# Performance work log

Measured on AMD Instinct MI355X. Metric: run time of the kernel, lower is better.

## Reference

```python
import jax, jax.numpy as jnp
import numpy as np

B, CIN, COUT, H, W = 16, 128, 128, 64, 64
E, PS, FF = 8, 16, 8
GC, HID, HC = 4 * FF, 64, COUT * 4  # gate_channel, gate hidden, bottleneck hidden


def conv(x, w, stride=1, pad=0, groups=1):
    # x: [B,C,H,W], w: [O,I/groups,kh,kw]
    return jax.lax.conv_general_dilated(
        x, w, (stride, stride), [(pad, pad), (pad, pad)], feature_group_count=groups)


def group_norm(x, scale, bias, groups, eps=1e-5):
    b, c = x.shape[:2]
    xr = x.reshape(b, groups, c // groups, *x.shape[2:])
    m = xr.mean(axis=(2, 3, 4), keepdims=True)
    v = xr.var(axis=(2, 3, 4), keepdims=True)
    xr = (xr - m) * jax.lax.rsqrt(v + eps)
    return xr.reshape(x.shape) * scale[None, :, None, None] + bias[None, :, None, None]


def setup_inputs() -> dict:
    key = jax.random.key(0)
    ks = jax.random.split(key, 8)
    f = lambda k, shp: jax.random.normal(k, shp, jnp.float32) * 0.05
    return dict(
        x=jax.random.normal(ks[0], (B, CIN, H, W), jnp.float32),
        w_exp=f(ks[1], (E, COUT, CIN, 3, 3)),
        gn_exp_s=jnp.ones((E, COUT), jnp.float32),
        gn_exp_b=jnp.zeros((E, COUT), jnp.float32),
        w1=f(ks[2], (GC, HID)), b1=jnp.zeros((HID,), jnp.float32),
        w2=f(ks[3], (HID, E)), b2=jnp.zeros((E,), jnp.float32),
        w_pw1=f(ks[4], (HC, COUT, 1, 1)),
        gn1_s=jnp.ones((HC,), jnp.float32), gn1_b=jnp.zeros((HC,), jnp.float32),
        w_dw=f(ks[5], (HC, 1, 3, 3)),
        gn2_s=jnp.ones((HC,), jnp.float32), gn2_b=jnp.zeros((HC,), jnp.float32),
        w_pw2=f(ks[6], (COUT, HC, 1, 1)),
        gn3_s=jnp.ones((COUT,), jnp.float32), gn3_b=jnp.zeros((COUT,), jnp.float32),
    )


def reference(x, w_exp, gn_exp_s, gn_exp_b, w1, b1, w2, b2,
              w_pw1, gn1_s, gn1_b, w_dw, gn2_s, gn2_b, w_pw2, gn3_s, gn3_b):
    # ---- Conv experts (residual 3x3 conv + GN + SiLU), vmapped over experts ----
    def expert(w, s, b):
        y = conv(x, w, pad=1)
        y = group_norm(y, s, b, groups=min(8, COUT))
        return jax.nn.silu(y) + x  # use_residual=True, CIN == COUT

    ys = jax.vmap(expert)(w_exp, gn_exp_s, gn_exp_b)  # [E,B,C,H,W]

    # ---- Router gate: Fourier features of patch-center coordinates ----
    ph, pw = H // PS, W // PS
    cy = (jnp.arange(ph, dtype=jnp.float32) + 0.5) / ph
    cx = (jnp.arange(pw, dtype=jnp.float32) + 0.5) / pw
    freqs = (2.0 ** jnp.arange(FF, dtype=jnp.float32)) * jnp.pi
    ay = cy[:, None] * freqs  # [ph,FF]
    ax = cx[:, None] * freqs  # [pw,FF]
    feats = jnp.concatenate([
        jnp.broadcast_to(jnp.sin(ay)[:, None, :], (ph, pw, FF)),
        jnp.broadcast_to(jnp.cos(ay)[:, None, :], (ph, pw, FF)),
        jnp.broadcast_to(jnp.sin(ax)[None, :, :], (ph, pw, FF)),
        jnp.broadcast_to(jnp.cos(ax)[None, :, :], (ph, pw, FF)),
    ], axis=-1)  # [ph,pw,4*FF] == gate_channel
    hgate = jax.nn.silu(feats @ w1 + b1)
    wts = jax.nn.softmax(hgate @ w2 + b2, axis=-1)  # [ph,pw,E]

    # ---- Patch-wise combine of expert outputs ----
    wmap = jnp.repeat(jnp.repeat(wts, PS, axis=0), PS, axis=1)  # [H,W,E]
    combined = jnp.einsum('ebchw,hwe->bchw', ys, wmap)

    # ---- Inverted bottleneck: 1x1 -> dw3x3 -> 1x1(stride2) with GN+SiLU ----
    h = jax.nn.silu(group_norm(conv(combined, w_pw1), gn1_s, gn1_b, groups=8))
    h = jax.nn.silu(group_norm(conv(h, w_dw, pad=1, groups=HC), gn2_s, gn2_b, groups=8))
    h = jax.nn.silu(group_norm(conv(h, w_pw2, stride=2), gn3_s, gn3_b, groups=8))
    return h  # [B, COUT, H//2, W//2]
```

## Files before the change

kernel.cpp:

```cpp
#include <hip/hip_runtime.h>
#include <hip/hip_bf16.h>


#define B_ 16
#define CIN_ 128
#define COUT_ 128
#define H_ 64
#define W_ 64
#define HW_ 4096
#define E_ 8
#define FF_ 8
#define GC_ 32
#define HID_ 64
#define HC_ 512

typedef __hip_bfloat16 bf16;
typedef __bf16 bf16x8 __attribute__((ext_vector_type(8)));
typedef float f32x4 __attribute__((ext_vector_type(4)));

__device__ __forceinline__ float siluf(float v) { return v / (1.f + __expf(-v)); }
__device__ __forceinline__ float bf2f(bf16 v) { return __bfloat162float(v); }
__device__ __forceinline__ bf16 f2bf(float v) { return __float2bfloat16(v); }

__global__ void gate_kernel(const float* __restrict__ w1, const float* __restrict__ b1,
                            const float* __restrict__ w2, const float* __restrict__ b2,
                            float* __restrict__ wts) {
  int p = threadIdx.x;
  if (p >= 16) return;
  int i = p >> 2, j = p & 3;
  float cy = (i + 0.5f) * 0.25f;
  float cx = (j + 0.5f) * 0.25f;
  float feats[GC_];
#pragma unroll
  for (int f = 0; f < FF_; ++f) {
    float fr = 3.14159265358979f * (float)(1 << f);
    float ay = cy * fr, ax = cx * fr;
    feats[f] = sinf(ay);
    feats[FF_ + f] = cosf(ay);
    feats[2 * FF_ + f] = sinf(ax);
    feats[3 * FF_ + f] = cosf(ax);
  }
  float hid[HID_];
  for (int k = 0; k < HID_; ++k) {
    float a = b1[k];
#pragma unroll
    for (int m = 0; m < GC_; ++m) a = fmaf(feats[m], w1[m * HID_ + k], a);
    hid[k] = siluf(a);
  }
  float lg[E_];
  float mx = -1e30f;
#pragma unroll
  for (int e = 0; e < E_; ++e) {
    float a = b2[e];
    for (int k = 0; k < HID_; ++k) a = fmaf(hid[k], w2[k * E_ + e], a);
    lg[e] = a;
    mx = fmaxf(mx, a);
  }
  float s = 0.f;
#pragma unroll
  for (int e = 0; e < E_; ++e) { lg[e] = __expf(lg[e] - mx); s += lg[e]; }
  float inv = 1.f / s;
#pragma unroll
  for (int e = 0; e < E_; ++e) wts[p * E_ + e] = lg[e] * inv;
}

__global__ __launch_bounds__(256) void xt_kernel(const float* __restrict__ x,
                                                 bf16* __restrict__ xT) {
  __shared__ float t[128][65];
  int b = blockIdx.x >> 6, h = blockIdx.x & 63;
  int tid = threadIdx.x;
  int w = tid & 63, c4 = tid >> 6;
  const float* xb = x + ((size_t)(b * 128) * 64 + h) * 64;
#pragma unroll 4
  for (int rep = 0; rep < 32; ++rep) {
    int ci = rep * 4 + c4;
    t[ci][w] = xb[(size_t)ci * HW_ + w];
  }
  __syncthreads();
  bf16* dst = xT + (size_t)(b * 64 + h) * 8192;
#pragma unroll 4
  for (int rep = 0; rep < 32; ++rep) {
    int o = rep * 256 + tid;
    int cg = o >> 9, w2 = (o >> 3) & 63, lo = o & 7;
    dst[o] = f2bf(t[cg * 8 + lo][w2]);
  }
}

__global__ void wt_kernel(const float* __restrict__ w_exp, bf16* __restrict__ wT) {
  int idx = blockIdx.x * 256 + threadIdx.x;
  if (idx >= 1179648) return;
  int lo = idx & 7;
  int co = (idx >> 3) & 127;
  int cg = (idx >> 10) & 15;
  int rest = idx >> 14;
  int tap = rest % 9, e = rest / 9;
  int ci = cg * 8 + lo;
  wT[idx] = f2bf(w_exp[(((size_t)(e * 128 + co) * 128 + ci) * 9) + tap]);
}

__global__ void wpT_kernel(const float* __restrict__ w_pw1, const float* __restrict__ w_pw2,
                           bf16* __restrict__ wp1T, bf16* __restrict__ wp2T) {
  int idx = blockIdx.x * 256 + threadIdx.x;
  if (idx < 65536) wp1T[idx] = f2bf(w_pw1[idx]);
  else if (idx < 131072) wp2T[idx - 65536] = f2bf(w_pw2[idx - 65536]);
}

__global__ __launch_bounds__(256, 2) void conv_mfma(
    const bf16* __restrict__ xT, const bf16* __restrict__ wT,
    float* __restrict__ statsE, bf16* __restrict__ ys) {
  __shared__ __align__(16) char xls[8 * 6144];
  __shared__ __align__(16) char wls[8 * 2048];
  __shared__ float red[4][8][2];

  int blk = blockIdx.x;
  int rt = blk & 15, b = (blk >> 4) & 15, e = blk >> 8;
  int tid = threadIdx.x, lane = tid & 63, wave = tid >> 6;
  int quad = lane >> 4, l15 = lane & 15;
  int h0 = rt * 4;
  int h_local = wave;

  f32x4 acc[8][4];
#pragma unroll
  for (int mt = 0; mt < 8; ++mt)
#pragma unroll
    for (int nt = 0; nt < 4; ++nt) acc[mt][nt] = (f32x4){0.f, 0.f, 0.f, 0.f};

  bf16x8 bz;
#pragma unroll
  for (int j = 0; j < 8; ++j) bz[j] = (__bf16)0.f;

  for (int half = 0; half < 2; ++half) {
    __syncthreads();
#pragma unroll
    for (int s = 0; s < 12; ++s) {
      int seg = wave * 12 + s;
      int cg = seg / 6, r = seg % 6;
      int h = h0 - 1 + r;
      char* ldst = xls + cg * 6144 + r * 1024 + lane * 16;
      if ((unsigned)h < 64u) {
        const uint4* g = (const uint4*)((const char*)xT +
            ((size_t)((b * 64 + h) * 16) + half * 8 + cg) * 1024) + lane;
        *(uint4*)ldst = *g;
      } else {
        *(uint4*)ldst = make_uint4(0u, 0u, 0u, 0u);
      }
    }
    for (int tap = 0; tap < 9; ++tap) {
      int dr = tap / 3, ds = tap % 3;
      __syncthreads();
#pragma unroll
      for (int s = 0; s < 4; ++s) {
        int seg = wave * 4 + s;
        int cg = seg >> 1, cb = seg & 1;
        const uint4* g = (const uint4*)((const char*)wT +
            ((size_t)(((e * 9 + tap) * 16) + half * 8 + cg) * 128 + cb * 64) * 16) + lane;
        *(uint4*)(wls + cg * 2048 + cb * 1024 + lane * 16) = *g;
      }
      __syncthreads();
      int r_local = h_local + dr;
#pragma unroll
      for (int kc = 0; kc < 2; ++kc) {
        int cgq = kc * 4 + quad;
        bf16x8 af[8];
#pragma unroll
        for (int mt = 0; mt < 8; ++mt)
          af[mt] = *(const bf16x8*)(wls + cgq * 2048 + (mt * 16 + l15) * 16);
        bf16x8 bfr[4];
#pragma unroll
        for (int nt = 0; nt < 4; ++nt) {
          int w = nt * 16 + l15;
          int wsrc = w + ds - 1;
          bool valid = (unsigned)wsrc < 64u;
          int wc = valid ? wsrc : 0;
          bf16x8 v = *(const bf16x8*)(xls + cgq * 6144 + (r_local * 64 + wc) * 16);
          bfr[nt] = valid ? v : bz;
        }
#pragma unroll
        for (int mt = 0; mt < 8; ++mt)
#pragma unroll
          for (int nt = 0; nt < 4; ++nt)
            acc[mt][nt] = __builtin_amdgcn_mfma_f32_16x16x32_bf16(
                af[mt], bfr[nt], acc[mt][nt], 0, 0, 0);
      }
    }
  }

  int hh = h0 + h_local;
  bf16* yb = ys + (size_t)((e * 16 + b) * 128) * 4096;
#pragma unroll
  for (int mt = 0; mt < 8; ++mt) {
    float s = 0.f, ss = 0.f;
#pragma unroll
    for (int nt = 0; nt < 4; ++nt) {
      int w = nt * 16 + l15;
      int pos = hh * 64 + w;
#pragma unroll
      for (int r = 0; r < 4; ++r) {
        float v = acc[mt][nt][r];
        s += v;
        ss += v * v;
        int co = mt * 16 + quad * 4 + r;
        yb[(size_t)co * 4096 + pos] = f2bf(v);
      }
    }
#pragma unroll
    for (int off = 32; off; off >>= 1) {
      s += __shfl_down(s, off, 64);
      ss += __shfl_down(ss, off, 64);
    }
    if (lane == 0) { red[wave][mt][0] = s; red[wave][mt][1] = ss; }
  }
  __syncthreads();
  if (tid < 16) {
    int g = tid >> 1, which = tid & 1;
    float t = red[0][g][which] + red[1][g][which] + red[2][g][which] + red[3][g][which];
    atomicAdd(&statsE[((e * 16 + b) * 8 + g) * 2 + which], t);
  }
}

__global__ void finalize_stats(float* __restrict__ st, int n, float inv) {
  int i = blockIdx.x * 256 + threadIdx.x;
  if (i >= n) return;
  float S = st[i * 2], SS = st[i * 2 + 1];
  float mean = S * inv;
  float var = SS * inv - mean * mean;
  st[i * 2] = mean;
  st[i * 2 + 1] = rsqrtf(var + 1e-5f);
}

__global__ __launch_bounds__(256) void combine_cl(
    const float* __restrict__ x, const bf16* __restrict__ ys,
    const float* __restrict__ st, const float* __restrict__ gns,
    const float* __restrict__ gnb, const float* __restrict__ wts,
    bf16* __restrict__ ccl) {
  __shared__ bf16 tile[64][132];
  int b = blockIdx.x >> 6, h = blockIdx.x & 63;
  int t = threadIdx.x;
  int w32 = t & 31, coq = t >> 5;
  float m_[8], r_[8];
#pragma unroll
  for (int e = 0; e < 8; ++e) {
    m_[e] = st[((e * 16 + b) * 8 + coq) * 2];
    r_[e] = st[((e * 16 + b) * 8 + coq) * 2 + 1];
  }
#pragma unroll
  for (int wt2 = 0; wt2 < 2; ++wt2) {
    int w = wt2 * 32 + w32;
    int pid = (h >> 4) * 4 + (w >> 4);
    int pos = h * 64 + w;
    float wt_[8];
#pragma unroll
    for (int e = 0; e < 8; ++e) wt_[e] = wts[pid * 8 + e];
    for (int coi = 0; coi < 16; ++coi) {
      int co = coq * 16 + coi;
      float v = x[((size_t)(b * 128 + co) << 12) + pos];
#pragma unroll
      for (int e = 0; e < 8; ++e) {
        float y = bf2f(ys[((size_t)((e * 16 + b) * 128 + co) << 12) + pos]);
        float yn = (y - m_[e]) * r_[e] * gns[e * 128 + co] + gnb[e * 128 + co];
        v += siluf(yn) * wt_[e];
      }
      tile[w][co] = f2bf(v);
    }
  }
  __syncthreads();
  int row = t >> 2, q = t & 3;
  char* dst = (char*)ccl + ((size_t)(b * 4096 + h * 64 + row)) * 256 + q * 64;
  const char* src = (const char*)&tile[row][0] + q * 64;
#pragma unroll
  for (int i = 0; i < 4; ++i)
    *(uint4*)(dst + i * 16) = *(const uint4*)(src + i * 16);
}

__global__ __launch_bounds__(256) void pw1_mfma(
    const bf16* __restrict__ ccl, const bf16* __restrict__ wp1T,
    bf16* __restrict__ h1cl, float* __restrict__ stats1) {
  __shared__ __align__(16) char ls[65536];
  __shared__ float red[4][2][2];
  char* als = ls;
  char* bls = ls + 32768;
  int blk = blockIdx.x;
  int ntile = blk & 511, mtile = blk >> 9;
  int n0 = ntile * 128, m0 = mtile * 128;
  int t = threadIdx.x, lane = t & 63, wave = t >> 6;
  int quad = lane >> 4, l15 = lane & 15;
  int b = n0 >> 12;

#pragma unroll
  for (int i = 0; i < 8; ++i) {
    int id = t + 256 * i;
    int r = id >> 4, c = id & 15;
    *(uint4*)(als + c * 2048 + r * 16) =
        *(const uint4*)((const char*)wp1T + (size_t)(m0 + r) * 256 + c * 16);
    *(uint4*)(bls + c * 2048 + r * 16) =
        *(const uint4*)((const char*)ccl + (size_t)(n0 + r) * 256 + c * 16);
  }
  __syncthreads();

  f32x4 acc[8][2];
#pragma unroll
  for (int mt = 0; mt < 8; ++mt)
#pragma unroll
    for (int nt = 0; nt < 2; ++nt) acc[mt][nt] = (f32x4){0.f, 0.f, 0.f, 0.f};

#pragma unroll
  for (int kc = 0; kc < 4; ++kc) {
    int cgq = kc * 4 + quad;
    bf16x8 af[8];
#pragma unroll
    for (int mt = 0; mt < 8; ++mt)
      af[mt] = *(const bf16x8*)(als + cgq * 2048 + (mt * 16 + l15) * 16);
    bf16x8 bfr[2];
#pragma unroll
    for (int nt = 0; nt < 2; ++nt)
      bfr[nt] = *(const bf16x8*)(bls + cgq * 2048 + (wave * 32 + nt * 16 + l15) * 16);
#pragma unroll
    for (int mt = 0; mt < 8; ++mt)
#pragma unroll
      for (int nt = 0; nt < 2; ++nt)
        acc[mt][nt] = __builtin_amdgcn_mfma_f32_16x16x32_bf16(
            af[mt], bfr[nt], acc[mt][nt], 0, 0, 0);
  }

  __syncthreads();
  float s[2] = {0.f, 0.f}, ss[2] = {0.f, 0.f};
  bf16* tile = (bf16*)ls;
#pragma unroll
  for (int mt = 0; mt < 8; ++mt) {
    int gi = mt >> 2;
#pragma unroll
    for (int nt = 0; nt < 2; ++nt) {
      int n = wave * 32 + nt * 16 + l15;
#pragma unroll
      for (int r = 0; r < 4; ++r) {
        float v = acc[mt][nt][r];
        s[gi] += v;
        ss[gi] += v * v;
        tile[n * 132 + mt * 16 + quad * 4 + r] = f2bf(v);
      }
    }
  }
#pragma unroll
  for (int gi = 0; gi < 2; ++gi) {
#pragma unroll
    for (int off = 32; off; off >>= 1) {
      s[gi] += __shfl_down(s[gi], off, 64);
      ss[gi] += __shfl_down(ss[gi], off, 64);
    }
  }
  if (lane == 0) {
    red[wave][0][0] = s[0]; red[wave][0][1] = ss[0];
    red[wave][1][0] = s[1]; red[wave][1][1] = ss[1];
  }
  __syncthreads();
  if (t < 4) {
    int gi = t >> 1, which = t & 1;
    float v = red[0][gi][which] + red[1][gi][which] + red[2][gi][which] + red[3][gi][which];
    atomicAdd(&stats1[(b * 8 + mtile * 2 + gi) * 2 + which], v);
  }
#pragma unroll
  for (int i = 0; i < 8; ++i) {
    int id = t + 256 * i;
    int r = id >> 4, q = id & 15;
    char* dst = (char*)h1cl + (size_t)(n0 + r) * 1024 + m0 * 2 + q * 16;
    const char* src = (const char*)tile + r * 264 + q * 16;
    *(uint4*)dst = *(const uint4*)src;
  }
}

__global__ __launch_bounds__(256) void dw_cl(
    const bf16* __restrict__ h1cl, const float* __restrict__ w_dw,
    const float* __restrict__ st1, const float* __restrict__ gs,
    const float* __restrict__ gb, bf16* __restrict__ h2cl,
    float* __restrict__ stats2) {
  __shared__ __align__(16) bf16 tile[18 * 66 * 16];
  __shared__ float red2[4][2];
  int blk = blockIdx.x;
  int ht = blk & 3, hcg = (blk >> 2) & 31, b = blk >> 7;
  int h0 = ht * 16;
  int hc0 = hcg * 16;
  int hcb = hcg >> 2;
  int t = threadIdx.x;

  float mean = st1[(b * 8 + hcb) * 2], rstd = st1[(b * 8 + hcb) * 2 + 1];
  float scale[16], shift[16];
#pragma unroll
  for (int j = 0; j < 16; ++j) {
    float g = gs[hc0 + j];
    scale[j] = rstd * g;
    shift[j] = gb[hc0 + j] - mean * rstd * g;
  }

  for (int i = 0; i < 5; ++i) {
    int idx = t + 256 * i;
    if (idx >= 1188) break;
    int row = idx / 66, wslot = idx - row * 66;
    int hh = h0 - 1 + row;
    int w = wslot - 1;
    int swz = (wslot >> 2) & 3;
    bf16* dst = tile + (row * 66 + wslot) * 16;
    if ((unsigned)hh < 64u && (unsigned)w < 64u) {
      const char* p = (const char*)h1cl + ((size_t)(b * 4096 + hh * 64 + w) * 512 + hc0) * 2;
      uint4 a0 = *(const uint4*)p;
      uint4 a1 = *(const uint4*)(p + 16);
      const bf16* pv = (const bf16*)&a0;
      const bf16* pv1 = (const bf16*)&a1;
      bf16 outv[16];
#pragma unroll
      for (int j = 0; j < 8; ++j)
        outv[j] = f2bf(siluf(bf2f(pv[j]) * scale[j] + shift[j]));
#pragma unroll
      for (int j = 0; j < 8; ++j)
        outv[8 + j] = f2bf(siluf(bf2f(pv1[j]) * scale[8 + j] + shift[8 + j]));
#pragma unroll
      for (int qq = 0; qq < 4; ++qq) {
        int ph = (qq + swz) & 3;
        *(uint2*)(dst + ph * 4) = *(const uint2*)(outv + qq * 4);
      }
    } else {
      *(uint4*)dst = make_uint4(0u, 0u, 0u, 0u);
      *(uint4*)(dst + 8) = make_uint4(0u, 0u, 0u, 0u);
    }
  }
  __syncthreads();

  int w = t & 63, q = t >> 6;
  float wv[9][4];
#pragma unroll
  for (int j = 0; j < 4; ++j) {
    int hc = hc0 + q * 4 + j;
#pragma unroll
    for (int tap = 0; tap < 9; ++tap) wv[tap][j] = w_dw[hc * 9 + tap];
  }

  f32x4 win[3][3];
  float acc_s = 0.f, acc_ss = 0.f;

  auto ld4 = [&](int r, int dwi) -> f32x4 {
    int slot = w + dwi;
    int ph = (q + (slot >> 2)) & 3;
    const bf16* p = tile + (r * 66 + slot) * 16 + ph * 4;
    uint2 u = *(const uint2*)p;
    const bf16* pb = (const bf16*)&u;
    return (f32x4){bf2f(pb[0]), bf2f(pb[1]), bf2f(pb[2]), bf2f(pb[3])};
  };

#pragma unroll
  for (int dwi = 0; dwi < 3; ++dwi) {
    win[0][dwi] = ld4(0, dwi);
    win[1][dwi] = ld4(1, dwi);
  }
#pragma unroll
  for (int orow = 0; orow < 16; ++orow) {
    int rnew = orow + 2;
    int ringn = rnew % 3;
#pragma unroll
    for (int dwi = 0; dwi < 3; ++dwi) win[ringn][dwi] = ld4(rnew, dwi);
    f32x4 acc = (f32x4){0.f, 0.f, 0.f, 0.f};
#pragma unroll
    for (int dr = 0; dr < 3; ++dr) {
      int ring = (orow + dr) % 3;
#pragma unroll
      for (int dwi = 0; dwi < 3; ++dwi) {
#pragma unroll
        for (int j = 0; j < 4; ++j)
          acc[j] = fmaf(win[ring][dwi][j], wv[dr * 3 + dwi][j], acc[j]);
      }
    }
#pragma unroll
    for (int j = 0; j < 4; ++j) { acc_s += acc[j]; acc_ss += acc[j] * acc[j]; }
    if (!(orow & 1) && !(w & 1)) {
      int hglob = h0 + orow;
      int pos2 = (hglob >> 1) * 32 + (w >> 1);
      bf16 tmp[4];
#pragma unroll
      for (int j = 0; j < 4; ++j) tmp[j] = f2bf(acc[j]);
      *(uint2*)((char*)h2cl + ((size_t)(b * 1024 + pos2) * 512 + hc0 + q * 4) * 2) =
          *(const uint2*)tmp;
    }
  }

#pragma unroll
  for (int off = 32; off; off >>= 1) {
    acc_s += __shfl_down(acc_s, off, 64);
    acc_ss += __shfl_down(acc_ss, off, 64);
  }
  int wave = t >> 6;
  if ((t & 63) == 0) { red2[wave][0] = acc_s; red2[wave][1] = acc_ss; }
  __syncthreads();
  if (t < 2) {
    float v = red2[0][t] + red2[1][t] + red2[2][t] + red2[3][t];
    atomicAdd(&stats2[(b * 8 + hcb) * 2 + t], v);
  }
}

__global__ void norm2_kernel(bf16* __restrict__ h2, const float* __restrict__ st2,
                             const float* __restrict__ gs, const float* __restrict__ gb) {
  int tg = blockIdx.x * 256 + threadIdx.x;
  int e8 = tg * 8;
  int hc0 = e8 & 511;
  int rest = e8 >> 9;
  int bq = rest >> 10;
  int g = hc0 >> 6;
  float mean = st2[(bq * 8 + g) * 2], rstd = st2[(bq * 8 + g) * 2 + 1];
  uint4 v = *(const uint4*)((const char*)h2 + (size_t)tg * 16);
  bf16* pv = (bf16*)&v;
  bf16 outv[8];
#pragma unroll
  for (int j = 0; j < 8; ++j) {
    float x = bf2f(pv[j]);
    x = (x - mean) * rstd * gs[hc0 + j] + gb[hc0 + j];
    outv[j] = f2bf(siluf(x));
  }
  *(uint4*)((char*)h2 + (size_t)tg * 16) = *(const uint4*)outv;
}

__global__ __launch_bounds__(256) void pw2_mfma(
    const bf16* __restrict__ h2n, const bf16* __restrict__ wp2T,
    float* __restrict__ h3, float* __restrict__ stats3) {
  __shared__ __align__(16) char als[2][8192];
  __shared__ __align__(16) char bls[2][4096];
  __shared__ float red[4][8][2];
  int blk = blockIdx.x;
  int n0 = blk * 64;
  int b = n0 >> 10, posb = n0 & 1023;
  int t = threadIdx.x, lane = t & 63, wave = t >> 6;
  int quad = lane >> 4, l15 = lane & 15;
  int wbase = wave * 16;

  f32x4 acc[8];
#pragma unroll
  for (int mt = 0; mt < 8; ++mt) acc[mt] = (f32x4){0.f, 0.f, 0.f, 0.f};

  {
#pragma unroll
    for (int i = 0; i < 2; ++i) {
      int id = t + 256 * i;
      int c4 = id >> 7, r = id & 127;
      *(uint4*)(als[0] + c4 * 2048 + r * 16) =
          *(const uint4*)((const char*)wp2T + (size_t)r * 1024 + c4 * 16);
    }
    int c4 = t >> 6, r = t & 63;
    *(uint4*)(bls[0] + c4 * 1024 + r * 16) =
        *(const uint4*)((const char*)h2n + (size_t)(n0 + r) * 1024 + c4 * 16);
  }
  for (int kc = 0; kc < 16; ++kc) {
    __syncthreads();
    if (kc + 1 < 16) {
      int nb = (kc + 1) & 1;
#pragma unroll
      for (int i = 0; i < 2; ++i) {
        int id = t + 256 * i;
        int c4 = id >> 7, r = id & 127;
        *(uint4*)(als[nb] + c4 * 2048 + r * 16) =
            *(const uint4*)((const char*)wp2T + (size_t)r * 1024 + ((kc + 1) * 4 + c4) * 16);
      }
      int c4 = t >> 6, r = t & 63;
      *(uint4*)(bls[nb] + c4 * 1024 + r * 16) =
          *(const uint4*)((const char*)h2n + (size_t)(n0 + r) * 1024 + ((kc + 1) * 4 + c4) * 16);
    }
    int buf = kc & 1;
    bf16x8 bf1 = *(const bf16x8*)(bls[buf] + quad * 1024 + (wbase + l15) * 16);
#pragma unroll
    for (int mt = 0; mt < 8; ++mt) {
      bf16x8 af = *(const bf16x8*)(als[buf] + quad * 2048 + (mt * 16 + l15) * 16);
      acc[mt] = __builtin_amdgcn_mfma_f32_16x16x32_bf16(af, bf1, acc[mt], 0, 0, 0);
    }
  }

#pragma unroll
  for (int mt = 0; mt < 8; ++mt) {
    float s = 0.f, ss = 0.f;
    int pos = posb + wbase + l15;
#pragma unroll
    for (int r = 0; r < 4; ++r) {
      float v = acc[mt][r];
      s += v;
      ss += v * v;
      int co = mt * 16 + quad * 4 + r;
      h3[(size_t)(b * 128 + co) * 1024 + pos] = v;
    }
#pragma unroll
    for (int off = 32; off; off >>= 1) {
      s += __shfl_down(s, off, 64);
      ss += __shfl_down(ss, off, 64);
    }
    if (lane == 0) { red[wave][mt][0] = s; red[wave][mt][1] = ss; }
  }
  __syncthreads();
  if (t < 16) {
    int mt = t >> 1, which = t & 1;
    float v = red[0][mt][which] + red[1][mt][which] + red[2][mt][which] + red[3][mt][which];
    atomicAdd(&stats3[(b * 8 + mt) * 2 + which], v);
  }
}

__global__ void out_kernel(const float* __restrict__ h3, const float* __restrict__ stats,
                           const float* __restrict__ gs, const float* __restrict__ gb,
                           float* __restrict__ out) {
  const int total = B_ * COUT_ * 1024;
  for (int idx = blockIdx.x * blockDim.x + threadIdx.x; idx < total; idx += gridDim.x * blockDim.x) {
    int c = (idx >> 10) & 127;
    int b = idx >> 17;
    int bg = b * 8 + (c >> 4);
    float S = stats[bg * 2], SS = stats[bg * 2 + 1];
    float mean = S * (1.f / 16384.f);
    float var = SS * (1.f / 16384.f) - mean * mean;
    float rstd = rsqrtf(var + 1e-5f);
    float v = (h3[idx] - mean) * rstd * gs[c] + gb[c];
    out[idx] = siluf(v);
  }
}

extern "C" void kernel_launch(void* const* d_in, const int* in_sizes, int n_in,
                              void* d_out, int out_size, void* d_ws, size_t ws_size,
                              hipStream_t stream) {
  const float* x = (const float*)d_in[0];
  const float* w_exp = (const float*)d_in[1];
  const float* gn_exp_s = (const float*)d_in[2];
  const float* gn_exp_b = (const float*)d_in[3];
  const float* w1 = (const float*)d_in[4];
  const float* b1 = (const float*)d_in[5];
  const float* w2 = (const float*)d_in[6];
  const float* b2 = (const float*)d_in[7];
  const float* w_pw1 = (const float*)d_in[8];
  const float* gn1_s = (const float*)d_in[9];
  const float* gn1_b = (const float*)d_in[10];
  const float* w_dw = (const float*)d_in[11];
  const float* gn2_s = (const float*)d_in[12];
  const float* gn2_b = (const float*)d_in[13];
  const float* w_pw2 = (const float*)d_in[14];
  const float* gn3_s = (const float*)d_in[15];
  const float* gn3_b = (const float*)d_in[16];

  char* ws = (char*)d_ws;
  const size_t WP1T_OFF = 16384;
  const size_t WP2T_OFF = WP1T_OFF + 131072;
  const size_t XT_OFF = WP2T_OFF + 131072;
  const size_t WT_OFF = XT_OFF + 16777216;
  const size_t YS_OFF = WT_OFF + 2359296;
  const size_t NEEDED = YS_OFF + 134217728;
  if (ws_size < NEEDED) return;

  float* wts = (float*)ws;
  float* stats1 = (float*)(ws + 1024);
  float* stats2 = (float*)(ws + 2048);
  float* stats3 = (float*)(ws + 3072);
  float* statsE = (float*)(ws + 4096);
  bf16* wp1T = (bf16*)(ws + WP1T_OFF);
  bf16* wp2T = (bf16*)(ws + WP2T_OFF);
  bf16* xT = (bf16*)(ws + XT_OFF);
  bf16* ccl = (bf16*)(ws + XT_OFF);
  bf16* wT = (bf16*)(ws + WT_OFF);
  bf16* ys = (bf16*)(ws + YS_OFF);
  bf16* h1cl = (bf16*)(ws + YS_OFF);
  bf16* h2cl = (bf16*)(ws + YS_OFF + 67108864);
  float* h3 = (float*)(ws + YS_OFF + 83886080);

  hipMemsetAsync(ws, 0, 16384, stream);
  gate_kernel<<<1, 64, 0, stream>>>(w1, b1, w2, b2, wts);
  xt_kernel<<<B_ * 64, 256, 0, stream>>>(x, xT);
  wt_kernel<<<4608, 256, 0, stream>>>(w_exp, wT);
  wpT_kernel<<<512, 256, 0, stream>>>(w_pw1, w_pw2, wp1T, wp2T);
  conv_mfma<<<E_ * B_ * 16, 256, 0, stream>>>(xT, wT, statsE, ys);
  finalize_stats<<<4, 256, 0, stream>>>(statsE, 1024, 1.f / 65536.f);
  combine_cl<<<B_ * 64, 256, 0, stream>>>(x, ys, statsE, gn_exp_s, gn_exp_b, wts, ccl);
  pw1_mfma<<<4 * 512, 256, 0, stream>>>(ccl, wp1T, h1cl, stats1);
  finalize_stats<<<1, 128, 0, stream>>>(stats1, 128, 1.f / 262144.f);
  dw_cl<<<B_ * 32 * 4, 256, 0, stream>>>(h1cl, w_dw, stats1, gn1_s, gn1_b, h2cl, stats2);
  finalize_stats<<<1, 128, 0, stream>>>(stats2, 128, 1.f / 262144.f);
  norm2_kernel<<<4096, 256, 0, stream>>>(h2cl, stats2, gn2_s, gn2_b);
  pw2_mfma<<<256, 256, 0, stream>>>(h2cl, wp2T, h3, stats3);
  out_kernel<<<1024, 256, 0, stream>>>(h3, stats3, gn3_s, gn3_b, (float*)d_out);
}
```

Measured before the change: 496.4 us.

## Switch expert conv to 32x32x16 MFMA with register-prefetched weights and async LDS loads

The expert 3x3 conv kernel now uses 32x32x16 bf16 MFMA tiles (4x2 per wave) in place of 16x16x32 tiles (8x4). This cuts the number of LDS fragment reads per MFMA and changes the accumulator register layout, so the GroupNorm statistics epilogue is remapped to the new output layout. Weights for the next tap are prefetched into registers while the current tap computes, and input rows are copied to LDS with global_load_lds instead of going through registers. The async copy is not followed by an explicit vmcnt wait before the barrier, which may be a correctness risk.

```diff
diff --git a/kernel.cpp b/kernel.cpp
--- a/kernel.cpp
+++ b/kernel.cpp
@@ -17,10 +17,17 @@
 typedef __hip_bfloat16 bf16;
 typedef __bf16 bf16x8 __attribute__((ext_vector_type(8)));
 typedef float f32x4 __attribute__((ext_vector_type(4)));
+typedef float f32x16 __attribute__((ext_vector_type(16)));
 
 __device__ __forceinline__ float siluf(float v) { return v / (1.f + __expf(-v)); }
 __device__ __forceinline__ float bf2f(bf16 v) { return __bfloat162float(v); }
 __device__ __forceinline__ bf16 f2bf(float v) { return __float2bfloat16(v); }
+
+__device__ __forceinline__ void async_copy16(void* lds, const void* g) {
+  __builtin_amdgcn_global_load_lds(
+      (const __attribute__((address_space(1))) unsigned int*)g,
+      (__attribute__((address_space(3))) unsigned int*)lds, 16, 0, 0);
+}
 
 __global__ void gate_kernel(const float* __restrict__ w1, const float* __restrict__ b1,
                             const float* __restrict__ w2, const float* __restrict__ b2,
@@ -115,19 +122,34 @@
   int blk = blockIdx.x;
   int rt = blk & 15, b = (blk >> 4) & 15, e = blk >> 8;
   int tid = threadIdx.x, lane = tid & 63, wave = tid >> 6;
-  int quad = lane >> 4, l15 = lane & 15;
+  int l31 = lane & 31, lh = lane >> 5;
   int h0 = rt * 4;
   int h_local = wave;
 
-  f32x4 acc[8][4];
-#pragma unroll
-  for (int mt = 0; mt < 8; ++mt)
-#pragma unroll
-    for (int nt = 0; nt < 4; ++nt) acc[mt][nt] = (f32x4){0.f, 0.f, 0.f, 0.f};
+  f32x16 acc[4][2];
+#pragma unroll
+  for (int mt = 0; mt < 4; ++mt)
+#pragma unroll
+    for (int nt = 0; nt < 2; ++nt)
+#pragma unroll
+      for (int r = 0; r < 16; ++r) acc[mt][nt][r] = 0.f;
 
   bf16x8 bz;
 #pragma unroll
   for (int j = 0; j < 8; ++j) bz[j] = (__bf16)0.f;
+
+  uint4 wr[4];
+  auto wload = [&](int ht2) {
+    int half = ht2 / 9, tap = ht2 - half * 9;
+#pragma unroll
+    for (int s = 0; s < 4; ++s) {
+      int seg = wave * 4 + s;
+      int cg = seg >> 1, cb = seg & 1;
+      wr[s] = *((const uint4*)((const char*)wT +
+          ((size_t)(((e * 9 + tap) * 16) + half * 8 + cg) * 128 + cb * 64) * 16) + lane);
+    }
+  };
+  wload(0);
 
   for (int half = 0; half < 2; ++half) {
     __syncthreads();
@@ -136,13 +158,13 @@
       int seg = wave * 12 + s;
       int cg = seg / 6, r = seg % 6;
       int h = h0 - 1 + r;
-      char* ldst = xls + cg * 6144 + r * 1024 + lane * 16;
+      char* ldst = xls + cg * 6144 + r * 1024;
       if ((unsigned)h < 64u) {
-        const uint4* g = (const uint4*)((const char*)xT +
-            ((size_t)((b * 64 + h) * 16) + half * 8 + cg) * 1024) + lane;
-        *(uint4*)ldst = *g;
+        const char* g = (const char*)xT +
+            ((size_t)((b * 64 + h) * 16) + half * 8 + cg) * 1024 + lane * 16;
+        async_copy16(ldst + lane * 16, g);
       } else {
-        *(uint4*)ldst = make_uint4(0u, 0u, 0u, 0u);
+        *(uint4*)(ldst + lane * 16) = make_uint4(0u, 0u, 0u, 0u);
       }
     }
     for (int tap = 0; tap < 9; ++tap) {
@@ -152,23 +174,23 @@
       for (int s = 0; s < 4; ++s) {
         int seg = wave * 4 + s;
         int cg = seg >> 1, cb = seg & 1;
-        const uint4* g = (const uint4*)((const char*)wT +
-            ((size_t)(((e * 9 + tap) * 16) + half * 8 + cg) * 128 + cb * 64) * 16) + lane;
-        *(uint4*)(wls + cg * 2048 + cb * 1024 + lane * 16) = *g;
-      }
+        *(uint4*)(wls + cg * 2048 + cb * 1024 + lane * 16) = wr[s];
+      }
+      int ht2 = half * 9 + tap + 1;
+      if (ht2 < 18) wload(ht2);
       __syncthreads();
       int r_local = h_local + dr;
 #pragma unroll
-      for (int kc = 0; kc < 2; ++kc) {
-        int cgq = kc * 4 + quad;
-        bf16x8 af[8];
-#pragma unroll
-        for (int mt = 0; mt < 8; ++mt)
-          af[mt] = *(const bf16x8*)(wls + cgq * 2048 + (mt * 16 + l15) * 16);
-        bf16x8 bfr[4];
-#pragma unroll
-        for (int nt = 0; nt < 4; ++nt) {
-          int w = nt * 16 + l15;
+      for (int kc = 0; kc < 4; ++kc) {
+        int cgq = kc * 2 + lh;
+        bf16x8 af[4];
+#pragma unroll
+        for (int mt = 0; mt < 4; ++mt)
+          af[mt] = *(const bf16x8*)(wls + cgq * 2048 + (mt * 32 + l31) * 16);
+        bf16x8 bfr[2];
+#pragma unroll
+        for (int nt = 0; nt < 2; ++nt) {
+          int w = nt * 32 + l31;
           int wsrc = w + ds - 1;
           bool valid = (unsigned)wsrc < 64u;
           int wc = valid ? wsrc : 0;
@@ -176,10 +198,10 @@
           bfr[nt] = valid ? v : bz;
         }
 #pragma unroll
-        for (int mt = 0; mt < 8; ++mt)
-#pragma unroll
-          for (int nt = 0; nt < 4; ++nt)
-            acc[mt][nt] = __builtin_amdgcn_mfma_f32_16x16x32_bf16(
+        for (int mt = 0; mt < 4; ++mt)
+#pragma unroll
+          for (int nt = 0; nt < 2; ++nt)
+            acc[mt][nt] = __builtin_amdgcn_mfma_f32_32x32x16_bf16(
                 af[mt], bfr[nt], acc[mt][nt], 0, 0, 0);
       }
     }
@@ -188,27 +210,35 @@
   int hh = h0 + h_local;
   bf16* yb = ys + (size_t)((e * 16 + b) * 128) * 4096;
 #pragma unroll
-  for (int mt = 0; mt < 8; ++mt) {
-    float s = 0.f, ss = 0.f;
-#pragma unroll
-    for (int nt = 0; nt < 4; ++nt) {
-      int w = nt * 16 + l15;
+  for (int mt = 0; mt < 4; ++mt) {
+    float s[2] = {0.f, 0.f}, ss[2] = {0.f, 0.f};
+#pragma unroll
+    for (int nt = 0; nt < 2; ++nt) {
+      int w = nt * 32 + l31;
       int pos = hh * 64 + w;
 #pragma unroll
-      for (int r = 0; r < 4; ++r) {
-        float v = acc[mt][nt][r];
-        s += v;
-        ss += v * v;
-        int co = mt * 16 + quad * 4 + r;
+      for (int reg = 0; reg < 16; ++reg) {
+        float v = acc[mt][nt][reg];
+        int gi = reg >> 3;
+        s[gi] += v;
+        ss[gi] += v * v;
+        int co = mt * 32 + (reg & 3) + 8 * (reg >> 2) + 4 * lh;
         yb[(size_t)co * 4096 + pos] = f2bf(v);
       }
     }
 #pragma unroll
     for (int off = 32; off; off >>= 1) {
-      s += __shfl_down(s, off, 64);
-      ss += __shfl_down(ss, off, 64);
-    }
-    if (lane == 0) { red[wave][mt][0] = s; red[wave][mt][1] = ss; }
+      s[0] += __shfl_down(s[0], off, 64);
+      ss[0] += __shfl_down(ss[0], off, 64);
+      s[1] += __shfl_down(s[1], off, 64);
+      ss[1] += __shfl_down(ss[1], off, 64);
+    }
+    if (lane == 0) {
+      red[wave][2 * mt][0] = s[0];
+      red[wave][2 * mt][1] = ss[0];
+      red[wave][2 * mt + 1][0] = s[1];
+      red[wave][2 * mt + 1][1] = ss[1];
+    }
   }
   __syncthreads();
   if (tid < 16) {
```

Result: slower. 568.3 us (+14.5%).

## Fuse GroupNorm2+SiLU into pw2 staging and prefetch conv weights into registers

Applied to the files above, without the earlier changes.

Removes the standalone norm2 kernel and applies the second GroupNorm affine and SiLU while staging activation tiles into shared memory in the pw2 GEMM. This saves a full read/write pass over the hidden tensor and a launch. Separately, the expert conv kernel now loads the next tap's weight slice into registers right after the barrier, so the global load overlaps with the MFMA work. The costs are extra registers in conv and redundant per-tile normalization arithmetic in pw2.

```diff
diff --git a/kernel.cpp b/kernel.cpp
--- a/kernel.cpp
+++ b/kernel.cpp
@@ -129,6 +129,19 @@
 #pragma unroll
   for (int j = 0; j < 8; ++j) bz[j] = (__bf16)0.f;
 
+  uint4 wr[4];
+  auto wload = [&](int ht2) {
+    int hf = ht2 / 9, tp = ht2 - hf * 9;
+#pragma unroll
+    for (int s = 0; s < 4; ++s) {
+      int seg = wave * 4 + s;
+      int cg = seg >> 1, cb = seg & 1;
+      wr[s] = *((const uint4*)((const char*)wT +
+          ((size_t)(((e * 9 + tp) * 16) + hf * 8 + cg) * 128 + cb * 64) * 16) + lane);
+    }
+  };
+  wload(0);
+
   for (int half = 0; half < 2; ++half) {
     __syncthreads();
 #pragma unroll
@@ -152,11 +165,11 @@
       for (int s = 0; s < 4; ++s) {
         int seg = wave * 4 + s;
         int cg = seg >> 1, cb = seg & 1;
-        const uint4* g = (const uint4*)((const char*)wT +
-            ((size_t)(((e * 9 + tap) * 16) + half * 8 + cg) * 128 + cb * 64) * 16) + lane;
-        *(uint4*)(wls + cg * 2048 + cb * 1024 + lane * 16) = *g;
+        *(uint4*)(wls + cg * 2048 + cb * 1024 + lane * 16) = wr[s];
       }
       __syncthreads();
+      int ht2 = half * 9 + tap + 1;
+      if (ht2 < 18) wload(ht2);
       int r_local = h_local + dr;
 #pragma unroll
       for (int kc = 0; kc < 2; ++kc) {
@@ -494,30 +507,11 @@
   }
 }
 
-__global__ void norm2_kernel(bf16* __restrict__ h2, const float* __restrict__ st2,
-                             const float* __restrict__ gs, const float* __restrict__ gb) {
-  int tg = blockIdx.x * 256 + threadIdx.x;
-  int e8 = tg * 8;
-  int hc0 = e8 & 511;
-  int rest = e8 >> 9;
-  int bq = rest >> 10;
-  int g = hc0 >> 6;
-  float mean = st2[(bq * 8 + g) * 2], rstd = st2[(bq * 8 + g) * 2 + 1];
-  uint4 v = *(const uint4*)((const char*)h2 + (size_t)tg * 16);
-  bf16* pv = (bf16*)&v;
-  bf16 outv[8];
-#pragma unroll
-  for (int j = 0; j < 8; ++j) {
-    float x = bf2f(pv[j]);
-    x = (x - mean) * rstd * gs[hc0 + j] + gb[hc0 + j];
-    outv[j] = f2bf(siluf(x));
-  }
-  *(uint4*)((char*)h2 + (size_t)tg * 16) = *(const uint4*)outv;
-}
-
 __global__ __launch_bounds__(256) void pw2_mfma(
-    const bf16* __restrict__ h2n, const bf16* __restrict__ wp2T,
-    float* __restrict__ h3, float* __restrict__ stats3) {
+    const bf16* __restrict__ h2raw, const bf16* __restrict__ wp2T,
+    const float* __restrict__ st2, const float* __restrict__ gs2,
+    const float* __restrict__ gb2, float* __restrict__ h3,
+    float* __restrict__ stats3) {
   __shared__ __align__(16) char als[2][8192];
   __shared__ __align__(16) char bls[2][4096];
   __shared__ float red[4][8][2];
@@ -532,6 +526,23 @@
 #pragma unroll
   for (int mt = 0; mt < 8; ++mt) acc[mt] = (f32x4){0.f, 0.f, 0.f, 0.f};
 
+  auto stageB = [&](int buf, int kc) {
+    int c4 = t >> 6, r = t & 63;
+    int hcb = (kc * 4 + c4) * 8;
+    int g = hcb >> 6;
+    float mean = st2[(b * 8 + g) * 2], rstd = st2[(b * 8 + g) * 2 + 1];
+    uint4 raw = *(const uint4*)((const char*)h2raw + (size_t)(n0 + r) * 1024 + (kc * 4 + c4) * 16);
+    const bf16* pv = (const bf16*)&raw;
+    bf16 outv[8];
+#pragma unroll
+    for (int j = 0; j < 8; ++j) {
+      float v = bf2f(pv[j]);
+      v = (v - mean) * rstd * gs2[hcb + j] + gb2[hcb + j];
+      outv[j] = f2bf(siluf(v));
+    }
+    *(uint4*)(bls[buf] + c4 * 1024 + r * 16) = *(const uint4*)outv;
+  };
+
   {
 #pragma unroll
     for (int i = 0; i < 2; ++i) {
@@ -540,9 +551,7 @@
       *(uint4*)(als[0] + c4 * 2048 + r * 16) =
           *(const uint4*)((const char*)wp2T + (size_t)r * 1024 + c4 * 16);
     }
-    int c4 = t >> 6, r = t & 63;
-    *(uint4*)(bls[0] + c4 * 1024 + r * 16) =
-        *(const uint4*)((const char*)h2n + (size_t)(n0 + r) * 1024 + c4 * 16);
+    stageB(0, 0);
   }
   for (int kc = 0; kc < 16; ++kc) {
     __syncthreads();
@@ -555,9 +564,7 @@
         *(uint4*)(als[nb] + c4 * 2048 + r * 16) =
             *(const uint4*)((const char*)wp2T + (size_t)r * 1024 + ((kc + 1) * 4 + c4) * 16);
       }
-      int c4 = t >> 6, r = t & 63;
-      *(uint4*)(bls[nb] + c4 * 1024 + r * 16) =
-          *(const uint4*)((const char*)h2n + (size_t)(n0 + r) * 1024 + ((kc + 1) * 4 + c4) * 16);
+      stageB(nb, kc + 1);
     }
     int buf = kc & 1;
     bf16x8 bf1 = *(const bf16x8*)(bls[buf] + quad * 1024 + (wbase + l15) * 16);
@@ -669,7 +676,6 @@
   finalize_stats<<<1, 128, 0, stream>>>(stats1, 128, 1.f / 262144.f);
   dw_cl<<<B_ * 32 * 4, 256, 0, stream>>>(h1cl, w_dw, stats1, gn1_s, gn1_b, h2cl, stats2);
   finalize_stats<<<1, 128, 0, stream>>>(stats2, 128, 1.f / 262144.f);
-  norm2_kernel<<<4096, 256, 0, stream>>>(h2cl, stats2, gn2_s, gn2_b);
-  pw2_mfma<<<256, 256, 0, stream>>>(h2cl, wp2T, h3, stats3);
+  pw2_mfma<<<256, 256, 0, stream>>>(h2cl, wp2T, stats2, gn2_s, gn2_b, h3, stats3);
   out_kernel<<<1024, 256, 0, stream>>>(h3, stats3, gn3_s, gn3_b, (float*)d_out);
 }
```

Result: slower. 572.7 us (+15.4%).
